# Kernel tuning notes

Measured on AMD Instinct MI355X. Metric: run time of the kernel, lower is better.

## Reference

```python
import jax, jax.numpy as jnp
import numpy as np

EMB = 1024
HEADS = 16
HEAD_DIM = EMB // HEADS
SEQ = 2048
BATCH = 2
EPS = 1e-5


def gelu_tanh(x):
    # 0.5*x*(1+tanh(sqrt(2/pi)*(x+0.044715*x^3)))
    c = jnp.sqrt(jnp.asarray(2.0 / jnp.pi, x.dtype))
    return 0.5 * x * (1.0 + jnp.tanh(c * (x + 0.044715 * x * x * x)))


def layernorm(x, scale, shift):
    mean = jnp.mean(x, axis=-1, keepdims=True)
    # torch var(unbiased=True) -> ddof=1
    var = jnp.var(x, axis=-1, keepdims=True, ddof=1)
    return scale * (x - mean) / jnp.sqrt(var + EPS) + shift


def setup_inputs() -> dict:
    key = jax.random.key(0)
    ks = jax.random.split(key, 12)
    s = 0.02
    d = {
        "x": jax.random.normal(ks[0], (BATCH, SEQ, EMB), jnp.float32),
        "Wq": jax.random.normal(ks[1], (EMB, EMB), jnp.float32) * s,
        "bq": jnp.zeros((EMB,), jnp.float32),
        "Wk": jax.random.normal(ks[2], (EMB, EMB), jnp.float32) * s,
        "bk": jnp.zeros((EMB,), jnp.float32),
        "Wv": jax.random.normal(ks[3], (EMB, EMB), jnp.float32) * s,
        "bv": jnp.zeros((EMB,), jnp.float32),
        "Wo": jax.random.normal(ks[4], (EMB, EMB), jnp.float32) * s,
        "bo": jnp.zeros((EMB,), jnp.float32),
        "W1": jax.random.normal(ks[5], (EMB, 4 * EMB), jnp.float32) * s,
        "b1": jnp.zeros((4 * EMB,), jnp.float32),
        "W2": jax.random.normal(ks[6], (4 * EMB, EMB), jnp.float32) * s,
        "b2": jnp.zeros((EMB,), jnp.float32),
        "ln1_scale": jnp.ones((EMB,), jnp.float32),
        "ln1_shift": jnp.zeros((EMB,), jnp.float32),
        "ln2_scale": jnp.ones((EMB,), jnp.float32),
        "ln2_shift": jnp.zeros((EMB,), jnp.float32),
    }
    return d


def reference(x, Wq, bq, Wk, bk, Wv, bv, Wo, bo, W1, b1, W2, b2,
              ln1_scale, ln1_shift, ln2_scale, ln2_shift):
    b, n, _ = x.shape

    # --- attention sub-block (pre-norm) ---
    h = layernorm(x, ln1_scale, ln1_shift)
    q = (h @ Wq + bq).reshape(b, n, HEADS, HEAD_DIM).transpose(0, 2, 1, 3)
    k = (h @ Wk + bk).reshape(b, n, HEADS, HEAD_DIM).transpose(0, 2, 1, 3)
    v = (h @ Wv + bv).reshape(b, n, HEADS, HEAD_DIM).transpose(0, 2, 1, 3)

    # explicit O(n^2) scores, as in the source
    scores = jnp.einsum("bhqd,bhkd->bhqk", q, k)
    causal = jnp.triu(jnp.ones((n, n), bool), k=1)  # True above diagonal -> masked
    scores = jnp.where(causal, -jnp.inf, scores)
    weights = jax.nn.softmax(scores / jnp.sqrt(jnp.asarray(HEAD_DIM, x.dtype)), axis=-1)
    ctx = jnp.einsum("bhqk,bhkd->bhqd", weights, v)
    ctx = ctx.transpose(0, 2, 1, 3).reshape(b, n, EMB)
    x = x + (ctx @ Wo + bo)  # dropout is identity (rate 0 / eval)

    # --- FFN sub-block (pre-norm) ---
    h = layernorm(x, ln2_scale, ln2_shift)
    h = gelu_tanh(h @ W1 + b1)
    x = x + (h @ W2 + b2)
    return x
```

## Files before the change

### kernel.cpp

```cpp
#include <hip/hip_runtime.h>
#include <hip/hip_bf16.h>

#define EMB 1024
#define SEQ 2048
#define BATCH 2
#define HEADS 16
#define HDIM 64
#define ROWS (BATCH*SEQ)

typedef __hip_bfloat16 bf16;
typedef __bf16 bf16x8 __attribute__((ext_vector_type(8)));
typedef float f32x4 __attribute__((ext_vector_type(4)));

#define AS1 __attribute__((address_space(1)))
#define AS3 __attribute__((address_space(3)))

__device__ __forceinline__ void load_lds16(const void* g, void* l) {
    __builtin_amdgcn_global_load_lds((const AS1 void*)g, (AS3 void*)l, 16, 0, 0);
}

__device__ __forceinline__ float gelu_f(float x) {
    float y = 1.5957691216057308f * (x + 0.044715f * x * x * x);
    return x / (1.0f + __expf(-y));
}

__global__ void transpose_cast_kernel(const float* __restrict__ in, bf16* __restrict__ out,
                                      int R, int C) {
    __shared__ bf16 tile[32][33];
    int tx = threadIdx.x, ty = threadIdx.y;
    int c0 = blockIdx.x * 32, r0 = blockIdx.y * 32;
    for (int i = ty; i < 32; i += 8)
        tile[i][tx] = (bf16)in[(size_t)(r0 + i) * C + c0 + tx];
    __syncthreads();
    for (int i = ty; i < 32; i += 8)
        out[(size_t)(c0 + i) * R + r0 + tx] = tile[tx][i];
}

__global__ void transpose_cast4_kernel(const float* __restrict__ w0, const float* __restrict__ w1,
                                       const float* __restrict__ w2, const float* __restrict__ w3,
                                       bf16* __restrict__ o0, bf16* __restrict__ o1,
                                       bf16* __restrict__ o2, bf16* __restrict__ o3) {
    __shared__ bf16 tile[32][33];
    int z = blockIdx.z;
    const float* in = (z == 0) ? w0 : (z == 1) ? w1 : (z == 2) ? w2 : w3;
    bf16* out = (z == 0) ? o0 : (z == 1) ? o1 : (z == 2) ? o2 : o3;
    int tx = threadIdx.x, ty = threadIdx.y;
    int c0 = blockIdx.x * 32, r0 = blockIdx.y * 32;
    for (int i = ty; i < 32; i += 8)
        tile[i][tx] = (bf16)in[(size_t)(r0 + i) * 1024 + c0 + tx];
    __syncthreads();
    for (int i = ty; i < 32; i += 8)
        out[(size_t)(c0 + i) * 1024 + r0 + tx] = tile[tx][i];
}

__global__ void transpose_v_kernel(const bf16* __restrict__ v, bf16* __restrict__ vt) {
    __shared__ bf16 tile[32][33];
    int tx = threadIdx.x, ty = threadIdx.y;
    int bh = blockIdx.z;
    const bf16* in = v + (size_t)(bh >> 4) * SEQ * EMB + (bh & 15) * HDIM;
    bf16* out = vt + (size_t)bh * HDIM * SEQ;
    int s0 = blockIdx.x * 32, d0 = blockIdx.y * 32;
    for (int i = ty; i < 32; i += 8)
        tile[i][tx] = in[(size_t)(s0 + i) * EMB + d0 + tx];
    __syncthreads();
    for (int i = ty; i < 32; i += 8)
        out[(size_t)(d0 + i) * SEQ + s0 + tx] = tile[tx][i];
}

__global__ __launch_bounds__(256) void layernorm_kernel(const float* __restrict__ x,
                                                        bf16* __restrict__ out,
                                                        const float* __restrict__ scale,
                                                        const float* __restrict__ shift) {
    int row = blockIdx.x;
    int t = threadIdx.x;
    const float* xr = x + (size_t)row * EMB;
    float v[4];
    float s = 0.f, s2 = 0.f;
#pragma unroll
    for (int i = 0; i < 4; i++) {
        v[i] = xr[t + 256 * i];
        s += v[i];
        s2 += v[i] * v[i];
    }
#pragma unroll
    for (int off = 32; off > 0; off >>= 1) {
        s += __shfl_down(s, off);
        s2 += __shfl_down(s2, off);
    }
    __shared__ float sh[8];
    __shared__ float stats[2];
    int lane = t & 63, wid = t >> 6;
    if (lane == 0) { sh[wid] = s; sh[wid + 4] = s2; }
    __syncthreads();
    if (t == 0) {
        float ts = sh[0] + sh[1] + sh[2] + sh[3];
        float ts2 = sh[4] + sh[5] + sh[6] + sh[7];
        float mean = ts / (float)EMB;
        float var = (ts2 - (float)EMB * mean * mean) / (float)(EMB - 1);
        stats[0] = mean;
        stats[1] = rsqrtf(var + 1e-5f);
    }
    __syncthreads();
    float mean = stats[0], inv = stats[1];
#pragma unroll
    for (int i = 0; i < 4; i++) {
        int c = t + 256 * i;
        float y = (v[i] - mean) * inv * scale[c] + shift[c];
        out[(size_t)row * EMB + c] = (bf16)y;
    }
}

__device__ __forceinline__ void swz64(int id, int& bx, int& by) {
    int xcd = id & 7, m = id >> 3;
    by = xcd + 8 * (m & 3) + 32 * (m >> 6);
    bx = (m >> 2) & 15;
}

__device__ __forceinline__ void stage_half(const bf16* g, bf16* lds, int tid, size_t rowK64) {
    load_lds16(g, lds + tid * 8);
    load_lds16(g + rowK64, lds + 4096 + tid * 8);
}

template <int ACT, int QKV>
__global__ __launch_bounds__(512, 2) void gemm256_kernel(
    const bf16* __restrict__ A, const bf16* __restrict__ BT,
    bf16* __restrict__ C0, bf16* __restrict__ C1, bf16* __restrict__ C2,
    const float* __restrict__ bias0, const float* __restrict__ bias1,
    const float* __restrict__ bias2, int N, int K) {
    __shared__ __align__(16) bf16 lA[4][128 * 64];
    __shared__ __align__(16) bf16 lB[4][128 * 64];
    const int tid = threadIdx.x;
    const int wave = tid >> 6, lane = tid & 63;
    const int an = lane & 15, aq = lane >> 4;
    const int wr = wave >> 2, wc = wave & 3;

    int id = blockIdx.x;
    int xcd = id & 7, m = id >> 3;
    int by = xcd * 2 + (m & 1);
    int bx = m >> 1;
    int m0 = by * 256, n0 = bx * 256;

    const int srow = tid >> 3;
    const int csw = ((tid & 7) ^ (srow & 7)) * 8;
    const bf16* Ag = A + (size_t)(m0 + srow) * K + csw;
    const bf16* Bg = BT + (size_t)(n0 + srow) * K + csw;
    const size_t rowK64 = (size_t)64 * K;
    const size_t rowK128 = (size_t)128 * K;

    stage_half(Bg, lB[0], tid, rowK64);
    stage_half(Bg + rowK128, lB[1], tid, rowK64);
    stage_half(Ag, lA[0], tid, rowK64);
    stage_half(Ag + rowK128, lA[1], tid, rowK64);
    stage_half(Bg + 64, lB[2], tid, rowK64);
    stage_half(Bg + rowK128 + 64, lB[3], tid, rowK64);
    asm volatile("s_waitcnt vmcnt(4)" ::: "memory");
    __builtin_amdgcn_s_barrier();

    f32x4 acc[8][4] = {};
    const int NT = K >> 6;
    const int lrB = (wc & 1) * 64;

    for (int t = 0; t < NT; ++t) {
        const bf16* As = lA[(2 * t + wr) & 3];
        const bf16* Bs = lB[(2 * t + (wc >> 1)) & 3];
        bf16x8 bfv[4][2];
#pragma unroll
        for (int p = 0; p < 4; ++p) {
            bf16x8 af[2][2];
            if (p == 0) {
#pragma unroll
                for (int j = 0; j < 4; ++j)
#pragma unroll
                    for (int kk = 0; kk < 2; ++kk) {
                        int r = lrB + 16 * j + an;
                        bfv[j][kk] = *(const bf16x8*)(Bs + r * 64 + ((kk * 4 + aq) ^ (r & 7)) * 8);
                    }
            }
#pragma unroll
            for (int ii = 0; ii < 2; ++ii)
#pragma unroll
                for (int kk = 0; kk < 2; ++kk) {
                    int r = 16 * (2 * p + ii) + an;
                    af[ii][kk] = *(const bf16x8*)(As + r * 64 + ((kk * 4 + aq) ^ (r & 7)) * 8);
                }
            if (p == 0) {
                if (t + 1 < NT)
                    stage_half(Ag + (size_t)(t + 1) * 64, lA[(2 * t + 2) & 3], tid, rowK64);
            } else if (p == 1) {
                if (t + 1 < NT)
                    stage_half(Ag + rowK128 + (size_t)(t + 1) * 64, lA[(2 * t + 3) & 3], tid, rowK64);
            } else if (p == 2) {
                if (t + 2 < NT)
                    stage_half(Bg + (size_t)(t + 2) * 64, lB[(2 * t + 4) & 3], tid, rowK64);
            } else {
                if (t + 2 < NT) {
                    stage_half(Bg + rowK128 + (size_t)(t + 2) * 64, lB[(2 * t + 5) & 3], tid, rowK64);
                    asm volatile("s_waitcnt vmcnt(4)" ::: "memory");
                } else {
                    asm volatile("s_waitcnt vmcnt(0)" ::: "memory");
                }
            }
            __builtin_amdgcn_s_barrier();
            asm volatile("s_waitcnt lgkmcnt(0)" ::: "memory");
            __builtin_amdgcn_s_setprio(1);
#pragma unroll
            for (int ii = 0; ii < 2; ++ii)
#pragma unroll
                for (int j = 0; j < 4; ++j)
#pragma unroll
                    for (int kk = 0; kk < 2; ++kk)
                        acc[2 * p + ii][j] = __builtin_amdgcn_mfma_f32_16x16x32_bf16(
                            af[ii][kk], bfv[j][kk], acc[2 * p + ii][j], 0, 0, 0);
            __builtin_amdgcn_s_setprio(0);
            __builtin_amdgcn_s_barrier();
        }
    }

#pragma unroll
    for (int j = 0; j < 4; ++j) {
        int col = n0 + wc * 64 + 16 * j + an;
        if (QKV == 0) {
            float bv = bias0[col];
#pragma unroll
            for (int i = 0; i < 8; ++i) {
#pragma unroll
                for (int r = 0; r < 4; ++r) {
                    int row = m0 + wr * 128 + 16 * i + aq * 4 + r;
                    float v = acc[i][j][r] + bv;
                    if (ACT == 1) v = gelu_f(v);
                    C0[(size_t)row * N + col] = (bf16)v;
                }
            }
        } else {
            int region = col >> 10, c = col & 1023;
            const float* bp = (region == 0) ? bias0 : (region == 1) ? bias1 : bias2;
            bf16* outp = (region == 0) ? C0 : (region == 1) ? C1 : C2;
            float scl = (region == 0) ? 0.125f : 1.0f;
            float bv = bp[c];
#pragma unroll
            for (int i = 0; i < 8; ++i) {
#pragma unroll
                for (int r = 0; r < 4; ++r) {
                    int row = m0 + wr * 128 + 16 * i + aq * 4 + r;
                    float v = (acc[i][j][r] + bv) * scl;
                    outp[(size_t)row * EMB + c] = (bf16)v;
                }
            }
        }
    }
}

template <int RES, int OUTF>
__global__ __launch_bounds__(256) void gemm64_kernel(const bf16* __restrict__ A,
                                                     const bf16* __restrict__ BT,
                                                     void* __restrict__ Cout,
                                                     const float* __restrict__ bias,
                                                     const float* __restrict__ res,
                                                     int M, int N, int K) {
    __shared__ __align__(16) bf16 lA[2][2][64 * 32];
    __shared__ __align__(16) bf16 lB[2][2][64 * 32];
    int tid = threadIdx.x;
    int wave = tid >> 6, lane = tid & 63;
    int bx, by;
    swz64(blockIdx.x, bx, by);
    int m0 = by * 64, n0 = bx * 64;
    int wm = (wave >> 1) * 32, wn = (wave & 1) * 32;
    f32x4 acc[2][2] = {};

    int srow = wave * 16 + (lane >> 2);
    int skc = (lane & 3) * 8;
    const bf16* Ag = A + (size_t)(m0 + srow) * K + skc;
    const bf16* Bg = BT + (size_t)(n0 + srow) * K + skc;
    size_t woff = (size_t)(wave * 16) * 32;

    const int an = lane & 15;
    const int ak = (lane >> 4) * 8;

    load_lds16(Ag, &lA[0][0][woff]);
    load_lds16(Ag + 32, &lA[0][1][woff]);
    load_lds16(Bg, &lB[0][0][woff]);
    load_lds16(Bg + 32, &lB[0][1][woff]);

    int nsteps = K >> 6;
    for (int t = 0; t < nsteps; t++) {
        int buf = t & 1;
        asm volatile("s_waitcnt vmcnt(0)" ::: "memory");
        __syncthreads();
        if (t + 1 < nsteps) {
            int k0 = (t + 1) * 64;
            load_lds16(Ag + k0, &lA[buf ^ 1][0][woff]);
            load_lds16(Ag + k0 + 32, &lA[buf ^ 1][1][woff]);
            load_lds16(Bg + k0, &lB[buf ^ 1][0][woff]);
            load_lds16(Bg + k0 + 32, &lB[buf ^ 1][1][woff]);
        }
#pragma unroll
        for (int h = 0; h < 2; h++) {
            bf16x8 af[2], bfv[2];
#pragma unroll
            for (int i = 0; i < 2; i++)
                af[i] = *(const bf16x8*)(&lA[buf][h][(wm + 16 * i + an) * 32 + ak]);
#pragma unroll
            for (int j = 0; j < 2; j++)
                bfv[j] = *(const bf16x8*)(&lB[buf][h][(wn + 16 * j + an) * 32 + ak]);
#pragma unroll
            for (int i = 0; i < 2; i++)
#pragma unroll
                for (int j = 0; j < 2; j++)
                    acc[i][j] = __builtin_amdgcn_mfma_f32_16x16x32_bf16(af[i], bfv[j], acc[i][j], 0, 0, 0);
        }
    }
#pragma unroll
    for (int j = 0; j < 2; j++) {
        int col = n0 + wn + 16 * j + an;
        float bv = bias[col];
#pragma unroll
        for (int i = 0; i < 2; i++) {
#pragma unroll
            for (int r = 0; r < 4; r++) {
                int row = m0 + wm + 16 * i + (lane >> 4) * 4 + r;
                float vx = acc[i][j][r] + bv;
                size_t idx = (size_t)row * N + col;
                if (RES == 2) vx += res[idx];
                if (OUTF == 0) ((bf16*)Cout)[idx] = (bf16)vx;
                else ((float*)Cout)[idx] = vx;
            }
        }
    }
}

__global__ __launch_bounds__(256, 4) void attn_kernel(const bf16* __restrict__ q,
                                                      const bf16* __restrict__ k,
                                                      const bf16* __restrict__ vt,
                                                      bf16* __restrict__ ctx) {
    __shared__ __align__(16) bf16 ksm[2][64 * 64];
    __shared__ __align__(16) bf16 vsm[2][64 * 64];
    __shared__ __align__(16) bf16 pbuf[4][16][40];
    int tid = threadIdx.x;
    int wave = tid >> 6, lane = tid & 63;
    int id = blockIdx.x;
    int bh = id >> 5;
    int bx = ((id & 31) + bh) & 31;
    int b = bh >> 4, h = bh & 15;
    int q0 = bx * 64 + wave * 16;
    const bf16* qp = q + (size_t)b * SEQ * EMB + h * HDIM;
    const bf16* kp = k + (size_t)b * SEQ * EMB + h * HDIM;
    const bf16* vp = vt + (size_t)bh * HDIM * SEQ;

    int an = lane & 15, aq = lane >> 4;

    bf16x8 qf0 = *(const bf16x8*)(qp + (size_t)(q0 + an) * EMB + aq * 8);
    bf16x8 qf1 = *(const bf16x8*)(qp + (size_t)(q0 + an) * EMB + 32 + aq * 8);
    f32x4 o[4] = {};
    float lp[4] = {0.f, 0.f, 0.f, 0.f};

    int srow0 = tid >> 3;
    int srow1 = srow0 + 32;
    int sc = tid & 7;
    const bf16* kg0 = kp + (size_t)srow0 * EMB + ((sc ^ (srow0 & 7)) * 8);
    const bf16* kg1 = kp + (size_t)srow1 * EMB + ((sc ^ (srow1 & 7)) * 8);
    const bf16* vg0 = vp + (size_t)srow0 * SEQ + ((sc ^ (srow0 & 7)) * 8);
    const bf16* vg1 = vp + (size_t)srow1 * SEQ + ((sc ^ (srow1 & 7)) * 8);

    int nsteps = bx + 1;

    load_lds16(kg0, ksm[0] + tid * 8);
    load_lds16(kg1, ksm[0] + (256 + tid) * 8);
    load_lds16(vg0, vsm[0] + tid * 8);
    load_lds16(vg1, vsm[0] + (256 + tid) * 8);
    asm volatile("s_waitcnt vmcnt(0)" ::: "memory");
    __syncthreads();

    auto step = [&](int t, bool last_) {
        int buf = t & 1;
        if (!last_) {
            size_t ko = (size_t)(t + 1) * 64 * EMB;
            int vo = (t + 1) * 64;
            load_lds16(kg0 + ko, ksm[buf ^ 1] + tid * 8);
            load_lds16(kg1 + ko, ksm[buf ^ 1] + (256 + tid) * 8);
            load_lds16(vg0 + vo, vsm[buf ^ 1] + tid * 8);
            load_lds16(vg1 + vo, vsm[buf ^ 1] + (256 + tid) * 8);
        }
        const bf16* kb = ksm[buf];
        const bf16* vb = vsm[buf];
        int kvbase = t * 64;
#pragma unroll
        for (int hh = 0; hh < 2; hh++) {
#pragma unroll
            for (int nbl = 0; nbl < 2; nbl++) {
                int nb = hh * 2 + nbl;
                int krow = nb * 16 + an;
                bf16x8 kfa = *(const bf16x8*)(kb + krow * 64 + ((aq ^ (an & 7)) * 8));
                bf16x8 kfb = *(const bf16x8*)(kb + krow * 64 + (((4 + aq) ^ (an & 7)) * 8));
                f32x4 s = {};
                s = __builtin_amdgcn_mfma_f32_16x16x32_bf16(qf0, kfa, s, 0, 0, 0);
                s = __builtin_amdgcn_mfma_f32_16x16x32_bf16(qf1, kfb, s, 0, 0, 0);
                int kvg = kvbase + nb * 16 + an;
#pragma unroll
                for (int r = 0; r < 4; r++) {
                    float p = __expf(s[r]);
                    if (last_ && (kvg > q0 + aq * 4 + r)) p = 0.f;
                    lp[r] += p;
                    pbuf[wave][aq * 4 + r][nbl * 16 + an] = (bf16)p;
                }
            }
            asm volatile("s_waitcnt lgkmcnt(0)" ::: "memory");
            bf16x8 pa = *(const bf16x8*)(&pbuf[wave][an][aq * 8]);
#pragma unroll
            for (int dt = 0; dt < 4; dt++) {
                int drow = dt * 16 + an;
                bf16x8 vf = *(const bf16x8*)(vb + drow * 64 + (((hh * 4 + aq) ^ (an & 7)) * 8));
                o[dt] = __builtin_amdgcn_mfma_f32_16x16x32_bf16(pa, vf, o[dt], 0, 0, 0);
            }
        }
        if (!last_) {
            asm volatile("s_waitcnt vmcnt(0)" ::: "memory");
            __syncthreads();
        }
    };

    for (int t = 0; t < nsteps - 1; t++) step(t, false);
    step(nsteps - 1, true);

#pragma unroll
    for (int r = 0; r < 4; r++) {
        float v = lp[r];
        v += __shfl_xor(v, 1);
        v += __shfl_xor(v, 2);
        v += __shfl_xor(v, 4);
        v += __shfl_xor(v, 8);
        lp[r] = v;
    }
#pragma unroll
    for (int dt = 0; dt < 4; dt++) {
#pragma unroll
        for (int r = 0; r < 4; r++) {
            int row = q0 + aq * 4 + r;
            int col = h * HDIM + dt * 16 + an;
            ctx[((size_t)b * SEQ + row) * EMB + col] = (bf16)(o[dt][r] / lp[r]);
        }
    }
}

extern "C" void kernel_launch(void* const* d_in, const int* in_sizes, int n_in,
                              void* d_out, int out_size, void* d_ws, size_t ws_size,
                              hipStream_t stream) {
    const float* x = (const float*)d_in[0];
    const float* Wq = (const float*)d_in[1];
    const float* bq = (const float*)d_in[2];
    const float* Wk = (const float*)d_in[3];
    const float* bk = (const float*)d_in[4];
    const float* Wv = (const float*)d_in[5];
    const float* bv = (const float*)d_in[6];
    const float* Wo = (const float*)d_in[7];
    const float* bo = (const float*)d_in[8];
    const float* W1 = (const float*)d_in[9];
    const float* b1 = (const float*)d_in[10];
    const float* W2 = (const float*)d_in[11];
    const float* b2 = (const float*)d_in[12];
    const float* ln1s = (const float*)d_in[13];
    const float* ln1b = (const float*)d_in[14];
    const float* ln2s = (const float*)d_in[15];
    const float* ln2b = (const float*)d_in[16];
    float* out = (float*)d_out;

    char* ws = (char*)d_ws;
    const size_t MB = 1ull << 20;
    bf16* WqT = (bf16*)(ws + 0 * MB);
    bf16* WkT = (bf16*)(ws + 2 * MB);
    bf16* WvT = (bf16*)(ws + 4 * MB);
    bf16* WoT = (bf16*)(ws + 6 * MB);
    bf16* W1T = (bf16*)(ws + 8 * MB);
    bf16* W2T = (bf16*)(ws + 16 * MB);
    bf16* hbuf = (bf16*)(ws + 24 * MB);
    bf16* qbuf = (bf16*)(ws + 32 * MB);
    bf16* kbuf = (bf16*)(ws + 40 * MB);
    bf16* vbuf = (bf16*)(ws + 48 * MB);
    bf16* vtb = (bf16*)(ws + 56 * MB);
    bf16* ctxb = (bf16*)(ws + 64 * MB);
    float* x1 = (float*)(ws + 72 * MB);
    bf16* hff = (bf16*)(ws + 32 * MB);

    dim3 tb(32, 8);
    transpose_cast4_kernel<<<dim3(32, 32, 4), tb, 0, stream>>>(Wq, Wk, Wv, Wo, WqT, WkT, WvT, WoT);
    transpose_cast_kernel<<<dim3(128, 32), tb, 0, stream>>>(W1, W1T, 1024, 4096);
    transpose_cast_kernel<<<dim3(32, 128), tb, 0, stream>>>(W2, W2T, 4096, 1024);

    layernorm_kernel<<<ROWS, 256, 0, stream>>>(x, hbuf, ln1s, ln1b);

    gemm256_kernel<0, 1><<<192, 512, 0, stream>>>(hbuf, WqT, qbuf, kbuf, vbuf,
                                                  bq, bk, bv, EMB, EMB);

    transpose_v_kernel<<<dim3(64, 2, 32), tb, 0, stream>>>(vbuf, vtb);

    attn_kernel<<<1024, 256, 0, stream>>>(qbuf, kbuf, vtb, ctxb);

    gemm64_kernel<2, 1><<<1024, 256, 0, stream>>>(ctxb, WoT, x1, bo, x, ROWS, EMB, EMB);

    layernorm_kernel<<<ROWS, 256, 0, stream>>>(x1, hbuf, ln2s, ln2b);

    gemm256_kernel<1, 0><<<256, 512, 0, stream>>>(hbuf, W1T, hff, nullptr, nullptr,
                                                  b1, nullptr, nullptr, 4 * EMB, EMB);

    gemm64_kernel<2, 1><<<1024, 256, 0, stream>>>(hff, W2T, out, b2, x1, ROWS, EMB, 4 * EMB);
}
```

Baseline: 354.4 us.

## Replace 64x64 residual GEMM with 128x128 swizzled-LDS pipelined GEMM

The two residual-add GEMMs (Wo projection and W2 down-projection) move from a 64x64-tile double-buffered kernel to a 128x128-tile kernel. Each wave now computes a 64x64 sub-tile. The new kernel uses an XOR-swizzled LDS layout to avoid bank conflicts, a 4-slot ring buffer with loads issued a step or two ahead and interleaved with the MFMA phases, and s_setprio around the MFMA bursts. Larger tiles raise arithmetic intensity per LDS load. The cost is that only 256 workgroups launch, which may underfill the CUs and lengthen the tail on the K=1024 GEMM.

```diff
diff --git a/kernel.cpp b/kernel.cpp
--- a/kernel.cpp
+++ b/kernel.cpp
@@ -108,12 +108,6 @@
         float y = (v[i] - mean) * inv * scale[c] + shift[c];
         out[(size_t)row * EMB + c] = (bf16)y;
     }
-}
-
-__device__ __forceinline__ void swz64(int id, int& bx, int& by) {
-    int xcd = id & 7, m = id >> 3;
-    by = xcd + 8 * (m & 3) + 32 * (m >> 6);
-    bx = (m >> 2) & 15;
 }
 
 __device__ __forceinline__ void stage_half(const bf16* g, bf16* lds, int tid, size_t rowK64) {
@@ -251,73 +245,108 @@
 }
 
 template <int RES, int OUTF>
-__global__ __launch_bounds__(256) void gemm64_kernel(const bf16* __restrict__ A,
-                                                     const bf16* __restrict__ BT,
-                                                     void* __restrict__ Cout,
-                                                     const float* __restrict__ bias,
-                                                     const float* __restrict__ res,
-                                                     int M, int N, int K) {
-    __shared__ __align__(16) bf16 lA[2][2][64 * 32];
-    __shared__ __align__(16) bf16 lB[2][2][64 * 32];
-    int tid = threadIdx.x;
-    int wave = tid >> 6, lane = tid & 63;
-    int bx, by;
-    swz64(blockIdx.x, bx, by);
-    int m0 = by * 64, n0 = bx * 64;
-    int wm = (wave >> 1) * 32, wn = (wave & 1) * 32;
-    f32x4 acc[2][2] = {};
-
-    int srow = wave * 16 + (lane >> 2);
-    int skc = (lane & 3) * 8;
-    const bf16* Ag = A + (size_t)(m0 + srow) * K + skc;
-    const bf16* Bg = BT + (size_t)(n0 + srow) * K + skc;
-    size_t woff = (size_t)(wave * 16) * 32;
-
-    const int an = lane & 15;
-    const int ak = (lane >> 4) * 8;
-
-    load_lds16(Ag, &lA[0][0][woff]);
-    load_lds16(Ag + 32, &lA[0][1][woff]);
-    load_lds16(Bg, &lB[0][0][woff]);
-    load_lds16(Bg + 32, &lB[0][1][woff]);
-
-    int nsteps = K >> 6;
-    for (int t = 0; t < nsteps; t++) {
-        int buf = t & 1;
-        asm volatile("s_waitcnt vmcnt(0)" ::: "memory");
-        __syncthreads();
-        if (t + 1 < nsteps) {
-            int k0 = (t + 1) * 64;
-            load_lds16(Ag + k0, &lA[buf ^ 1][0][woff]);
-            load_lds16(Ag + k0 + 32, &lA[buf ^ 1][1][woff]);
-            load_lds16(Bg + k0, &lB[buf ^ 1][0][woff]);
-            load_lds16(Bg + k0 + 32, &lB[buf ^ 1][1][woff]);
-        }
-#pragma unroll
-        for (int h = 0; h < 2; h++) {
-            bf16x8 af[2], bfv[2];
-#pragma unroll
-            for (int i = 0; i < 2; i++)
-                af[i] = *(const bf16x8*)(&lA[buf][h][(wm + 16 * i + an) * 32 + ak]);
-#pragma unroll
-            for (int j = 0; j < 2; j++)
-                bfv[j] = *(const bf16x8*)(&lB[buf][h][(wn + 16 * j + an) * 32 + ak]);
-#pragma unroll
-            for (int i = 0; i < 2; i++)
-#pragma unroll
-                for (int j = 0; j < 2; j++)
-                    acc[i][j] = __builtin_amdgcn_mfma_f32_16x16x32_bf16(af[i], bfv[j], acc[i][j], 0, 0, 0);
-        }
-    }
-#pragma unroll
-    for (int j = 0; j < 2; j++) {
-        int col = n0 + wn + 16 * j + an;
+__global__ __launch_bounds__(256, 2) void gemm128_kernel(
+    const bf16* __restrict__ A, const bf16* __restrict__ BT,
+    void* __restrict__ Cout, const float* __restrict__ bias,
+    const float* __restrict__ res, int N, int K) {
+    __shared__ __align__(16) bf16 lA[4][64 * 64];
+    __shared__ __align__(16) bf16 lB[4][64 * 64];
+    const int tid = threadIdx.x;
+    const int wave = tid >> 6, lane = tid & 63;
+    const int an = lane & 15, aq = lane >> 4;
+    const int wr = wave >> 1, wc = wave & 1;
+
+    int id = blockIdx.x;
+    int xcd = id & 7, m = id >> 3;
+    int by = xcd * 4 + (m & 3);
+    int bx = m >> 2;
+    int m0 = by * 128, n0 = bx * 128;
+
+    const int srow = tid >> 3;
+    const int csw = ((tid & 7) ^ (srow & 7)) * 8;
+    const bf16* Ag = A + (size_t)(m0 + srow) * K + csw;
+    const bf16* Bg = BT + (size_t)(n0 + srow) * K + csw;
+    const size_t rowK32 = (size_t)32 * K;
+    const size_t rowK64 = (size_t)64 * K;
+
+    auto stage64 = [&](const bf16* g, bf16* lds) {
+        load_lds16(g, lds + tid * 8);
+        load_lds16(g + rowK32, lds + 2048 + tid * 8);
+    };
+
+    stage64(Bg, lB[0]);
+    stage64(Bg + rowK64, lB[1]);
+    stage64(Ag, lA[0]);
+    stage64(Ag + rowK64, lA[1]);
+    stage64(Bg + 64, lB[2]);
+    stage64(Bg + rowK64 + 64, lB[3]);
+    asm volatile("s_waitcnt vmcnt(4)" ::: "memory");
+    __builtin_amdgcn_s_barrier();
+
+    f32x4 acc[4][4] = {};
+    const int NT = K >> 6;
+
+    for (int t = 0; t < NT; ++t) {
+        const bf16* As = lA[(2 * t + wr) & 3];
+        const bf16* Bs = lB[(2 * t + wc) & 3];
+        bf16x8 bfv[4][2];
+#pragma unroll
+        for (int p = 0; p < 4; ++p) {
+            bf16x8 af[2];
+            if (p == 0) {
+#pragma unroll
+                for (int j = 0; j < 4; ++j)
+#pragma unroll
+                    for (int kk = 0; kk < 2; ++kk) {
+                        int r = 16 * j + an;
+                        bfv[j][kk] = *(const bf16x8*)(Bs + r * 64 + ((kk * 4 + aq) ^ (r & 7)) * 8);
+                    }
+            }
+#pragma unroll
+            for (int kk = 0; kk < 2; ++kk) {
+                int r = 16 * p + an;
+                af[kk] = *(const bf16x8*)(As + r * 64 + ((kk * 4 + aq) ^ (r & 7)) * 8);
+            }
+            if (p == 0) {
+                if (t + 1 < NT)
+                    stage64(Ag + (size_t)(t + 1) * 64, lA[(2 * t + 2) & 3]);
+            } else if (p == 1) {
+                if (t + 1 < NT)
+                    stage64(Ag + rowK64 + (size_t)(t + 1) * 64, lA[(2 * t + 3) & 3]);
+            } else if (p == 2) {
+                if (t + 2 < NT)
+                    stage64(Bg + (size_t)(t + 2) * 64, lB[(2 * t + 4) & 3]);
+            } else {
+                if (t + 2 < NT) {
+                    stage64(Bg + rowK64 + (size_t)(t + 2) * 64, lB[(2 * t + 5) & 3]);
+                    asm volatile("s_waitcnt vmcnt(4)" ::: "memory");
+                } else {
+                    asm volatile("s_waitcnt vmcnt(0)" ::: "memory");
+                }
+            }
+            __builtin_amdgcn_s_barrier();
+            asm volatile("s_waitcnt lgkmcnt(0)" ::: "memory");
+            __builtin_amdgcn_s_setprio(1);
+#pragma unroll
+            for (int j = 0; j < 4; ++j)
+#pragma unroll
+                for (int kk = 0; kk < 2; ++kk)
+                    acc[p][j] = __builtin_amdgcn_mfma_f32_16x16x32_bf16(
+                        af[kk], bfv[j][kk], acc[p][j], 0, 0, 0);
+            __builtin_amdgcn_s_setprio(0);
+            __builtin_amdgcn_s_barrier();
+        }
+    }
+
+#pragma unroll
+    for (int j = 0; j < 4; ++j) {
+        int col = n0 + wc * 64 + 16 * j + an;
         float bv = bias[col];
 #pragma unroll
-        for (int i = 0; i < 2; i++) {
-#pragma unroll
-            for (int r = 0; r < 4; r++) {
-                int row = m0 + wm + 16 * i + (lane >> 4) * 4 + r;
+        for (int i = 0; i < 4; ++i) {
+#pragma unroll
+            for (int r = 0; r < 4; ++r) {
+                int row = m0 + wr * 64 + 16 * i + aq * 4 + r;
                 float vx = acc[i][j][r] + bv;
                 size_t idx = (size_t)row * N + col;
                 if (RES == 2) vx += res[idx];
@@ -494,12 +523,12 @@
 
     attn_kernel<<<1024, 256, 0, stream>>>(qbuf, kbuf, vtb, ctxb);
 
-    gemm64_kernel<2, 1><<<1024, 256, 0, stream>>>(ctxb, WoT, x1, bo, x, ROWS, EMB, EMB);
+    gemm128_kernel<2, 1><<<256, 256, 0, stream>>>(ctxb, WoT, x1, bo, x, EMB, EMB);
 
     layernorm_kernel<<<ROWS, 256, 0, stream>>>(x1, hbuf, ln2s, ln2b);
 
     gemm256_kernel<1, 0><<<256, 512, 0, stream>>>(hbuf, W1T, hff, nullptr, nullptr,
                                                   b1, nullptr, nullptr, 4 * EMB, EMB);
 
-    gemm64_kernel<2, 1><<<1024, 256, 0, stream>>>(hff, W2T, out, b2, x1, ROWS, EMB, 4 * EMB);
-}
+    gemm128_kernel<2, 1><<<256, 256, 0, stream>>>(hff, W2T, out, b2, x1, EMB, 4 * EMB);
+}
```

Measured after the change: 391.4 us. +10.4%, slower.

## Replace final FFN down-projection GEMM with split-K 256x256 tiled kernel using atomics

Applied to the files above, without the earlier changes.

The W2 GEMM (K=4096) moves from a 64x64-tile kernel with 1024 blocks to a 256x256-tile MFMA kernel. K is split into four 1024-wide slices, and each slice atomically adds its partial sums into the fp32 output. The first slice also adds bias and residual. The larger tiles raise operand reuse, and the kernel uses a deeper LDS prefetch pipeline with XCD-aware block mapping. The cost is atomic traffic on the output, and correctness depends on the output buffer being zeroed before each launch.

```diff
diff --git a/kernel.cpp b/kernel.cpp
--- a/kernel.cpp
+++ b/kernel.cpp
@@ -245,6 +245,122 @@
                     float v = (acc[i][j][r] + bv) * scl;
                     outp[(size_t)row * EMB + c] = (bf16)v;
                 }
+            }
+        }
+    }
+}
+
+__global__ __launch_bounds__(512, 2) void gemm256sk_kernel(
+    const bf16* __restrict__ A, const bf16* __restrict__ BT,
+    float* __restrict__ out, const float* __restrict__ bias,
+    const float* __restrict__ res) {
+    const int KF = 4096;
+    const int KS = 1024;
+    const int N = 1024;
+    __shared__ __align__(16) bf16 lA[4][128 * 64];
+    __shared__ __align__(16) bf16 lB[4][128 * 64];
+    const int tid = threadIdx.x;
+    const int wave = tid >> 6, lane = tid & 63;
+    const int an = lane & 15, aq = lane >> 4;
+    const int wr = wave >> 2, wc = wave & 3;
+
+    int id = blockIdx.x;
+    int split = id >> 6;
+    int t6 = id & 63;
+    int xcd = t6 & 7, m = t6 >> 3;
+    int by = xcd * 2 + (m & 1);
+    int bx = m >> 1;
+    int m0 = by * 256, n0 = bx * 256;
+
+    const int srow = tid >> 3;
+    const int csw = ((tid & 7) ^ (srow & 7)) * 8;
+    const bf16* Ag = A + (size_t)(m0 + srow) * KF + split * KS + csw;
+    const bf16* Bg = BT + (size_t)(n0 + srow) * KF + split * KS + csw;
+    const size_t rowK64 = (size_t)64 * KF;
+    const size_t rowK128 = (size_t)128 * KF;
+
+    stage_half(Bg, lB[0], tid, rowK64);
+    stage_half(Bg + rowK128, lB[1], tid, rowK64);
+    stage_half(Ag, lA[0], tid, rowK64);
+    stage_half(Ag + rowK128, lA[1], tid, rowK64);
+    stage_half(Bg + 64, lB[2], tid, rowK64);
+    stage_half(Bg + rowK128 + 64, lB[3], tid, rowK64);
+    asm volatile("s_waitcnt vmcnt(4)" ::: "memory");
+    __builtin_amdgcn_s_barrier();
+
+    f32x4 acc[8][4] = {};
+    const int NT = KS >> 6;
+    const int lrB = (wc & 1) * 64;
+
+    for (int t = 0; t < NT; ++t) {
+        const bf16* As = lA[(2 * t + wr) & 3];
+        const bf16* Bs = lB[(2 * t + (wc >> 1)) & 3];
+        bf16x8 bfv[4][2];
+#pragma unroll
+        for (int p = 0; p < 4; ++p) {
+            bf16x8 af[2][2];
+            if (p == 0) {
+#pragma unroll
+                for (int j = 0; j < 4; ++j)
+#pragma unroll
+                    for (int kk = 0; kk < 2; ++kk) {
+                        int r = lrB + 16 * j + an;
+                        bfv[j][kk] = *(const bf16x8*)(Bs + r * 64 + ((kk * 4 + aq) ^ (r & 7)) * 8);
+                    }
+            }
+#pragma unroll
+            for (int ii = 0; ii < 2; ++ii)
+#pragma unroll
+                for (int kk = 0; kk < 2; ++kk) {
+                    int r = 16 * (2 * p + ii) + an;
+                    af[ii][kk] = *(const bf16x8*)(As + r * 64 + ((kk * 4 + aq) ^ (r & 7)) * 8);
+                }
+            if (p == 0) {
+                if (t + 1 < NT)
+                    stage_half(Ag + (size_t)(t + 1) * 64, lA[(2 * t + 2) & 3], tid, rowK64);
+            } else if (p == 1) {
+                if (t + 1 < NT)
+                    stage_half(Ag + rowK128 + (size_t)(t + 1) * 64, lA[(2 * t + 3) & 3], tid, rowK64);
+            } else if (p == 2) {
+                if (t + 2 < NT)
+                    stage_half(Bg + (size_t)(t + 2) * 64, lB[(2 * t + 4) & 3], tid, rowK64);
+            } else {
+                if (t + 2 < NT) {
+                    stage_half(Bg + rowK128 + (size_t)(t + 2) * 64, lB[(2 * t + 5) & 3], tid, rowK64);
+                    asm volatile("s_waitcnt vmcnt(4)" ::: "memory");
+                } else {
+                    asm volatile("s_waitcnt vmcnt(0)" ::: "memory");
+                }
+            }
+            __builtin_amdgcn_s_barrier();
+            asm volatile("s_waitcnt lgkmcnt(0)" ::: "memory");
+            __builtin_amdgcn_s_setprio(1);
+#pragma unroll
+            for (int ii = 0; ii < 2; ++ii)
+#pragma unroll
+                for (int j = 0; j < 4; ++j)
+#pragma unroll
+                    for (int kk = 0; kk < 2; ++kk)
+                        acc[2 * p + ii][j] = __builtin_amdgcn_mfma_f32_16x16x32_bf16(
+                            af[ii][kk], bfv[j][kk], acc[2 * p + ii][j], 0, 0, 0);
+            __builtin_amdgcn_s_setprio(0);
+            __builtin_amdgcn_s_barrier();
+        }
+    }
+
+#pragma unroll
+    for (int j = 0; j < 4; ++j) {
+        int col = n0 + wc * 64 + 16 * j + an;
+        float bv = bias[col];
+#pragma unroll
+        for (int i = 0; i < 8; ++i) {
+#pragma unroll
+            for (int r = 0; r < 4; ++r) {
+                int row = m0 + wr * 128 + 16 * i + aq * 4 + r;
+                size_t idx = (size_t)row * N + col;
+                float v = acc[i][j][r];
+                if (split == 0) v += bv + res[idx];
+                unsafeAtomicAdd(&out[idx], v);
             }
         }
     }
@@ -501,5 +617,5 @@
     gemm256_kernel<1, 0><<<256, 512, 0, stream>>>(hbuf, W1T, hff, nullptr, nullptr,
                                                   b1, nullptr, nullptr, 4 * EMB, EMB);
 
-    gemm64_kernel<2, 1><<<1024, 256, 0, stream>>>(hff, W2T, out, b2, x1, ROWS, EMB, 4 * EMB);
-}
+    gemm256sk_kernel<<<256, 512, 0, stream>>>(hff, W2T, out, b2, x1);
+}
```

Measured after the change: 407.8 us. 1.15x slower.

## Replace 256x256 and 64x64 GEMMs with a unified 128x64 tiled GEMM kernel

Applied to the files above, without the earlier changes.

Removes the large 256x256 eight-wave GEMM with its 4-stage LDS pipeline and the small 64x64 GEMM. All four projections (QKV, Wo, W1, W2) now use a single templated 128x64-tile kernel with double buffering and fused bias/GELU/residual epilogues. This gives more blocks for occupancy on the big GEMMs and more reuse on the small ones. In exchange, the big GEMMs lose the deep pipelining and the larger-tile data reuse, and the LDS reads are unswizzled.

```diff
diff --git a/kernel.cpp b/kernel.cpp
--- a/kernel.cpp
+++ b/kernel.cpp
@@ -110,162 +110,28 @@
     }
 }
 
-__device__ __forceinline__ void swz64(int id, int& bx, int& by) {
-    int xcd = id & 7, m = id >> 3;
-    by = xcd + 8 * (m & 3) + 32 * (m >> 6);
-    bx = (m >> 2) & 15;
-}
-
-__device__ __forceinline__ void stage_half(const bf16* g, bf16* lds, int tid, size_t rowK64) {
-    load_lds16(g, lds + tid * 8);
-    load_lds16(g + rowK64, lds + 4096 + tid * 8);
-}
-
-template <int ACT, int QKV>
-__global__ __launch_bounds__(512, 2) void gemm256_kernel(
-    const bf16* __restrict__ A, const bf16* __restrict__ BT,
-    bf16* __restrict__ C0, bf16* __restrict__ C1, bf16* __restrict__ C2,
-    const float* __restrict__ bias0, const float* __restrict__ bias1,
-    const float* __restrict__ bias2, int N, int K) {
-    __shared__ __align__(16) bf16 lA[4][128 * 64];
-    __shared__ __align__(16) bf16 lB[4][128 * 64];
-    const int tid = threadIdx.x;
-    const int wave = tid >> 6, lane = tid & 63;
-    const int an = lane & 15, aq = lane >> 4;
-    const int wr = wave >> 2, wc = wave & 3;
-
-    int id = blockIdx.x;
-    int xcd = id & 7, m = id >> 3;
-    int by = xcd * 2 + (m & 1);
-    int bx = m >> 1;
-    int m0 = by * 256, n0 = bx * 256;
-
-    const int srow = tid >> 3;
-    const int csw = ((tid & 7) ^ (srow & 7)) * 8;
-    const bf16* Ag = A + (size_t)(m0 + srow) * K + csw;
-    const bf16* Bg = BT + (size_t)(n0 + srow) * K + csw;
-    const size_t rowK64 = (size_t)64 * K;
-    const size_t rowK128 = (size_t)128 * K;
-
-    stage_half(Bg, lB[0], tid, rowK64);
-    stage_half(Bg + rowK128, lB[1], tid, rowK64);
-    stage_half(Ag, lA[0], tid, rowK64);
-    stage_half(Ag + rowK128, lA[1], tid, rowK64);
-    stage_half(Bg + 64, lB[2], tid, rowK64);
-    stage_half(Bg + rowK128 + 64, lB[3], tid, rowK64);
-    asm volatile("s_waitcnt vmcnt(4)" ::: "memory");
-    __builtin_amdgcn_s_barrier();
-
-    f32x4 acc[8][4] = {};
-    const int NT = K >> 6;
-    const int lrB = (wc & 1) * 64;
-
-    for (int t = 0; t < NT; ++t) {
-        const bf16* As = lA[(2 * t + wr) & 3];
-        const bf16* Bs = lB[(2 * t + (wc >> 1)) & 3];
-        bf16x8 bfv[4][2];
-#pragma unroll
-        for (int p = 0; p < 4; ++p) {
-            bf16x8 af[2][2];
-            if (p == 0) {
-#pragma unroll
-                for (int j = 0; j < 4; ++j)
-#pragma unroll
-                    for (int kk = 0; kk < 2; ++kk) {
-                        int r = lrB + 16 * j + an;
-                        bfv[j][kk] = *(const bf16x8*)(Bs + r * 64 + ((kk * 4 + aq) ^ (r & 7)) * 8);
-                    }
-            }
-#pragma unroll
-            for (int ii = 0; ii < 2; ++ii)
-#pragma unroll
-                for (int kk = 0; kk < 2; ++kk) {
-                    int r = 16 * (2 * p + ii) + an;
-                    af[ii][kk] = *(const bf16x8*)(As + r * 64 + ((kk * 4 + aq) ^ (r & 7)) * 8);
-                }
-            if (p == 0) {
-                if (t + 1 < NT)
-                    stage_half(Ag + (size_t)(t + 1) * 64, lA[(2 * t + 2) & 3], tid, rowK64);
-            } else if (p == 1) {
-                if (t + 1 < NT)
-                    stage_half(Ag + rowK128 + (size_t)(t + 1) * 64, lA[(2 * t + 3) & 3], tid, rowK64);
-            } else if (p == 2) {
-                if (t + 2 < NT)
-                    stage_half(Bg + (size_t)(t + 2) * 64, lB[(2 * t + 4) & 3], tid, rowK64);
-            } else {
-                if (t + 2 < NT) {
-                    stage_half(Bg + rowK128 + (size_t)(t + 2) * 64, lB[(2 * t + 5) & 3], tid, rowK64);
-                    asm volatile("s_waitcnt vmcnt(4)" ::: "memory");
-                } else {
-                    asm volatile("s_waitcnt vmcnt(0)" ::: "memory");
-                }
-            }
-            __builtin_amdgcn_s_barrier();
-            asm volatile("s_waitcnt lgkmcnt(0)" ::: "memory");
-            __builtin_amdgcn_s_setprio(1);
-#pragma unroll
-            for (int ii = 0; ii < 2; ++ii)
-#pragma unroll
-                for (int j = 0; j < 4; ++j)
-#pragma unroll
-                    for (int kk = 0; kk < 2; ++kk)
-                        acc[2 * p + ii][j] = __builtin_amdgcn_mfma_f32_16x16x32_bf16(
-                            af[ii][kk], bfv[j][kk], acc[2 * p + ii][j], 0, 0, 0);
-            __builtin_amdgcn_s_setprio(0);
-            __builtin_amdgcn_s_barrier();
-        }
-    }
-
-#pragma unroll
-    for (int j = 0; j < 4; ++j) {
-        int col = n0 + wc * 64 + 16 * j + an;
-        if (QKV == 0) {
-            float bv = bias0[col];
-#pragma unroll
-            for (int i = 0; i < 8; ++i) {
-#pragma unroll
-                for (int r = 0; r < 4; ++r) {
-                    int row = m0 + wr * 128 + 16 * i + aq * 4 + r;
-                    float v = acc[i][j][r] + bv;
-                    if (ACT == 1) v = gelu_f(v);
-                    C0[(size_t)row * N + col] = (bf16)v;
-                }
-            }
-        } else {
-            int region = col >> 10, c = col & 1023;
-            const float* bp = (region == 0) ? bias0 : (region == 1) ? bias1 : bias2;
-            bf16* outp = (region == 0) ? C0 : (region == 1) ? C1 : C2;
-            float scl = (region == 0) ? 0.125f : 1.0f;
-            float bv = bp[c];
-#pragma unroll
-            for (int i = 0; i < 8; ++i) {
-#pragma unroll
-                for (int r = 0; r < 4; ++r) {
-                    int row = m0 + wr * 128 + 16 * i + aq * 4 + r;
-                    float v = (acc[i][j][r] + bv) * scl;
-                    outp[(size_t)row * EMB + c] = (bf16)v;
-                }
-            }
-        }
-    }
-}
-
-template <int RES, int OUTF>
-__global__ __launch_bounds__(256) void gemm64_kernel(const bf16* __restrict__ A,
-                                                     const bf16* __restrict__ BT,
-                                                     void* __restrict__ Cout,
-                                                     const float* __restrict__ bias,
-                                                     const float* __restrict__ res,
-                                                     int M, int N, int K) {
-    __shared__ __align__(16) bf16 lA[2][2][64 * 32];
+template <int ACT, int QKV, int RES, int OUTF>
+__global__ __launch_bounds__(256) void gemm12864_kernel(const bf16* __restrict__ A,
+                                                        const bf16* __restrict__ BT,
+                                                        void* __restrict__ C0,
+                                                        void* __restrict__ C1,
+                                                        void* __restrict__ C2,
+                                                        const float* __restrict__ bias0,
+                                                        const float* __restrict__ bias1,
+                                                        const float* __restrict__ bias2,
+                                                        const float* __restrict__ res,
+                                                        int N, int K) {
+    __shared__ __align__(16) bf16 lA[2][2][128 * 32];
     __shared__ __align__(16) bf16 lB[2][2][64 * 32];
     int tid = threadIdx.x;
     int wave = tid >> 6, lane = tid & 63;
-    int bx, by;
-    swz64(blockIdx.x, bx, by);
-    int m0 = by * 64, n0 = bx * 64;
-    int wm = (wave >> 1) * 32, wn = (wave & 1) * 32;
-    f32x4 acc[2][2] = {};
+    int id = blockIdx.x;
+    int xcd = id & 7, m = id >> 3;
+    int by = xcd + 8 * (m & 3);
+    int bx = m >> 2;
+    int m0 = by * 128, n0 = bx * 64;
+    int wm = (wave >> 1) * 64, wn = (wave & 1) * 32;
+    f32x4 acc[4][2] = {};
 
     int srow = wave * 16 + (lane >> 2);
     int skc = (lane & 3) * 8;
@@ -275,9 +141,12 @@
 
     const int an = lane & 15;
     const int ak = (lane >> 4) * 8;
+    const size_t rowK64 = (size_t)64 * K;
 
     load_lds16(Ag, &lA[0][0][woff]);
+    load_lds16(Ag + rowK64, &lA[0][0][woff + 64 * 32]);
     load_lds16(Ag + 32, &lA[0][1][woff]);
+    load_lds16(Ag + rowK64 + 32, &lA[0][1][woff + 64 * 32]);
     load_lds16(Bg, &lB[0][0][woff]);
     load_lds16(Bg + 32, &lB[0][1][woff]);
 
@@ -289,21 +158,23 @@
         if (t + 1 < nsteps) {
             int k0 = (t + 1) * 64;
             load_lds16(Ag + k0, &lA[buf ^ 1][0][woff]);
+            load_lds16(Ag + rowK64 + k0, &lA[buf ^ 1][0][woff + 64 * 32]);
             load_lds16(Ag + k0 + 32, &lA[buf ^ 1][1][woff]);
+            load_lds16(Ag + rowK64 + k0 + 32, &lA[buf ^ 1][1][woff + 64 * 32]);
             load_lds16(Bg + k0, &lB[buf ^ 1][0][woff]);
             load_lds16(Bg + k0 + 32, &lB[buf ^ 1][1][woff]);
         }
 #pragma unroll
         for (int h = 0; h < 2; h++) {
-            bf16x8 af[2], bfv[2];
-#pragma unroll
-            for (int i = 0; i < 2; i++)
+            bf16x8 af[4], bfv[2];
+#pragma unroll
+            for (int i = 0; i < 4; i++)
                 af[i] = *(const bf16x8*)(&lA[buf][h][(wm + 16 * i + an) * 32 + ak]);
 #pragma unroll
             for (int j = 0; j < 2; j++)
                 bfv[j] = *(const bf16x8*)(&lB[buf][h][(wn + 16 * j + an) * 32 + ak]);
 #pragma unroll
-            for (int i = 0; i < 2; i++)
+            for (int i = 0; i < 4; i++)
 #pragma unroll
                 for (int j = 0; j < 2; j++)
                     acc[i][j] = __builtin_amdgcn_mfma_f32_16x16x32_bf16(af[i], bfv[j], acc[i][j], 0, 0, 0);
@@ -312,17 +183,35 @@
 #pragma unroll
     for (int j = 0; j < 2; j++) {
         int col = n0 + wn + 16 * j + an;
-        float bv = bias[col];
-#pragma unroll
-        for (int i = 0; i < 2; i++) {
-#pragma unroll
-            for (int r = 0; r < 4; r++) {
-                int row = m0 + wm + 16 * i + (lane >> 4) * 4 + r;
-                float vx = acc[i][j][r] + bv;
-                size_t idx = (size_t)row * N + col;
-                if (RES == 2) vx += res[idx];
-                if (OUTF == 0) ((bf16*)Cout)[idx] = (bf16)vx;
-                else ((float*)Cout)[idx] = vx;
+        if (QKV == 0) {
+            float bv = bias0[col];
+#pragma unroll
+            for (int i = 0; i < 4; i++) {
+#pragma unroll
+                for (int r = 0; r < 4; r++) {
+                    int row = m0 + wm + 16 * i + (lane >> 4) * 4 + r;
+                    float vx = acc[i][j][r] + bv;
+                    if (ACT == 1) vx = gelu_f(vx);
+                    size_t idx = (size_t)row * N + col;
+                    if (RES == 2) vx += res[idx];
+                    if (OUTF == 0) ((bf16*)C0)[idx] = (bf16)vx;
+                    else ((float*)C0)[idx] = vx;
+                }
+            }
+        } else {
+            int region = col >> 10, c = col & 1023;
+            const float* bp = (region == 0) ? bias0 : (region == 1) ? bias1 : bias2;
+            bf16* outp = (region == 0) ? (bf16*)C0 : (region == 1) ? (bf16*)C1 : (bf16*)C2;
+            float scl = (region == 0) ? 0.125f : 1.0f;
+            float bv = bp[c];
+#pragma unroll
+            for (int i = 0; i < 4; i++) {
+#pragma unroll
+                for (int r = 0; r < 4; r++) {
+                    int row = m0 + wm + 16 * i + (lane >> 4) * 4 + r;
+                    float vx = (acc[i][j][r] + bv) * scl;
+                    outp[(size_t)row * EMB + c] = (bf16)vx;
+                }
             }
         }
     }
@@ -487,19 +376,21 @@
 
     layernorm_kernel<<<ROWS, 256, 0, stream>>>(x, hbuf, ln1s, ln1b);
 
-    gemm256_kernel<0, 1><<<192, 512, 0, stream>>>(hbuf, WqT, qbuf, kbuf, vbuf,
-                                                  bq, bk, bv, EMB, EMB);
+    gemm12864_kernel<0, 1, 0, 0><<<1536, 256, 0, stream>>>(
+        hbuf, WqT, qbuf, kbuf, vbuf, bq, bk, bv, nullptr, 3 * EMB, EMB);
 
     transpose_v_kernel<<<dim3(64, 2, 32), tb, 0, stream>>>(vbuf, vtb);
 
     attn_kernel<<<1024, 256, 0, stream>>>(qbuf, kbuf, vtb, ctxb);
 
-    gemm64_kernel<2, 1><<<1024, 256, 0, stream>>>(ctxb, WoT, x1, bo, x, ROWS, EMB, EMB);
+    gemm12864_kernel<0, 0, 2, 1><<<512, 256, 0, stream>>>(
+        ctxb, WoT, x1, nullptr, nullptr, bo, nullptr, nullptr, x, EMB, EMB);
 
     layernorm_kernel<<<ROWS, 256, 0, stream>>>(x1, hbuf, ln2s, ln2b);
 
-    gemm256_kernel<1, 0><<<256, 512, 0, stream>>>(hbuf, W1T, hff, nullptr, nullptr,
-                                                  b1, nullptr, nullptr, 4 * EMB, EMB);
-
-    gemm64_kernel<2, 1><<<1024, 256, 0, stream>>>(hff, W2T, out, b2, x1, ROWS, EMB, 4 * EMB);
-}
+    gemm12864_kernel<1, 0, 0, 0><<<2048, 256, 0, stream>>>(
+        hbuf, W1T, hff, nullptr, nullptr, b1, nullptr, nullptr, nullptr, 4 * EMB, EMB);
+
+    gemm12864_kernel<0, 0, 2, 1><<<512, 256, 0, stream>>>(
+        hff, W2T, out, nullptr, nullptr, b2, nullptr, nullptr, x1, EMB, 4 * EMB);
+}
```

Result: slower. 366.3 us (+3.3%).
